# Optimization experiments

Measured on AMD Instinct MI355X. Metric: run time of the kernel, lower is better.

Reference implementation:

```python
import jax, jax.numpy as jnp
import numpy as np

B_SZ, L, D_MODEL = 2, 2048, 2048
INTER, HEADS, P, N, G, K = 4096, 64, 64, 128, 1, 4
CONV_DIM = INTER + 2 * G * N
EPS = 1e-5


def silu(x):
    return x * jax.nn.sigmoid(x)


def softplus_thresh(x, threshold=10.0):
    # matches source: where(x < thr, log(1+exp(x)), x)
    return jnp.where(x < threshold, jnp.log1p(jnp.exp(jnp.minimum(x, threshold))), x)


def setup_inputs() -> dict:
    key = jax.random.key(0)
    ks = jax.random.split(key, 8)
    s = 0.02
    return {
        "hidden_states": jax.random.normal(ks[0], (B_SZ, L, D_MODEL), jnp.float32),
        "W_z": jax.random.normal(ks[1], (D_MODEL, INTER), jnp.float32) * s,
        "W_xBC": jax.random.normal(ks[2], (D_MODEL, CONV_DIM), jnp.float32) * s,
        "W_dt": jax.random.normal(ks[3], (D_MODEL, HEADS), jnp.float32) * s,
        "conv_w": jax.random.normal(ks[4], (CONV_DIM, K), jnp.float32) * 0.1,
        "conv_b": jnp.zeros((CONV_DIM,), jnp.float32),
        "dt_bias": jax.random.uniform(ks[5], (HEADS,), jnp.float32, -2.0, 0.0),
        "A_log": jnp.log(jnp.arange(1, HEADS + 1, dtype=jnp.float32)),
        "D": jnp.ones((HEADS,), jnp.float32),
        "norm_w": jnp.ones((INTER,), jnp.float32),
        "W_out": jax.random.normal(ks[6], (INTER, D_MODEL), jnp.float32) * s,
    }


def reference(hidden_states, W_z, W_xBC, W_dt, conv_w, conv_b, dt_bias, A_log, D, norm_w, W_out):
    b, l, _ = hidden_states.shape
    Hg = HEADS // G  # heads per group

    gate = hidden_states @ W_z                      # [b,l,INTER]
    xBC = hidden_states @ W_xBC                     # [b,l,CONV_DIM]
    dt = softplus_thresh(hidden_states @ W_dt + dt_bias)  # [b,l,H]

    # causal depthwise conv1d + silu (padding=K-1, truncated to seq_len)
    xp = jnp.pad(xBC, ((0, 0), (K - 1, 0), (0, 0)))
    kern = jnp.transpose(conv_w)[:, None, :]        # [K,1,CONV_DIM] (WIO)
    xBC = jax.lax.conv_general_dilated(
        xp, kern, (1,), 'VALID',
        dimension_numbers=('NWC', 'WIO', 'NWC'),
        feature_group_count=CONV_DIM)
    xBC = silu(xBC + conv_b)

    gns = G * N
    x = xBC[..., :INTER].reshape(b, l, G, Hg, P)
    Bm = xBC[..., INTER:INTER + gns].reshape(b, l, G, N)
    Cm = xBC[..., INTER + gns:].reshape(b, l, G, N)

    A = -jnp.exp(A_log)                             # [H]
    dA = jnp.exp(dt * A).reshape(b, l, G, Hg)       # [b,l,G,Hg]
    dtx = dt.reshape(b, l, G, Hg)[..., None] * x    # [b,l,G,Hg,P]

    def step(state, inp):
        dA_t, dtx_t, B_t, C_t = inp
        # state: [b,G,Hg,P,N]
        state = state * dA_t[..., None, None] + dtx_t[..., None] * B_t[:, :, None, None, :]
        y_t = jnp.einsum('bghpn,bgn->bghp', state, C_t)
        return state, y_t

    xs = (jnp.moveaxis(dA, 1, 0), jnp.moveaxis(dtx, 1, 0),
          jnp.moveaxis(Bm, 1, 0), jnp.moveaxis(Cm, 1, 0))
    state0 = jnp.zeros((b, G, Hg, P, N), jnp.float32)
    _, ys = jax.lax.scan(step, state0, xs)          # [l,b,G,Hg,P]
    y = jnp.moveaxis(ys, 0, 1) + D.reshape(G, Hg)[..., None] * x
    scan_out = y.reshape(b, l, INTER)

    # gated RMSNorm within groups
    hs = scan_out.reshape(b, l, G, INTER // G).astype(jnp.float32)
    gt = gate.reshape(b, l, G, INTER // G).astype(jnp.float32)
    hs = hs * silu(gt)
    var = jnp.mean(hs * hs, axis=-1, keepdims=True)
    hs = hs * jax.lax.rsqrt(var + EPS)
    normed = norm_w * hs.reshape(b, l, INTER)

    return normed @ W_out
```

## Files before the change

### kernel.cpp

```cpp
#include <hip/hip_runtime.h>
#include <hip/hip_bf16.h>
#include <math.h>

typedef unsigned short u16;
typedef unsigned int   u32;
typedef __attribute__((ext_vector_type(8))) short short8;
typedef __attribute__((ext_vector_type(4))) float f32x4;

#define B_SZ     2
#define LSEQ     2048
#define DMODEL   2048
#define INTER    4096
#define HEADS    64
#define NSTATE   128
#define CONV_DIM 4352
#define XSTR     8576
#define NMAIN    8192
#define NTAILC   512
#define NTAILS   384
#define EPS      1e-5f
#define QCH      64
#define NCHUNK   (LSEQ / QCH)

__device__ __forceinline__ float bf2f(u16 u) {
    u32 v = ((u32)u) << 16;
    return __builtin_bit_cast(float, v);
}
__device__ __forceinline__ u16 f2bf(float x) {
    __hip_bfloat16 h = __float2bfloat16(x);
    return __builtin_bit_cast(u16, h);
}
__device__ __forceinline__ u32 pack2(float lo, float hi) {
    return (u32)f2bf(lo) | ((u32)f2bf(hi) << 16);
}
__device__ __forceinline__ void gl2lds16(const void* g, void* l) {
    __builtin_amdgcn_global_load_lds(
        (const __attribute__((address_space(1))) u32*)g,
        (__attribute__((address_space(3))) u32*)l, 16, 0, 0);
}

__global__ __launch_bounds__(256) void cvt_f32_bf16(
    const float* __restrict__ in, u16* __restrict__ out, int n4)
{
    int i = blockIdx.x * 256 + threadIdx.x;
    if (i >= n4) return;
    float4 v = ((const float4*)in)[i];
    ushort4 o;
    o.x = f2bf(v.x); o.y = f2bf(v.y); o.z = f2bf(v.z); o.w = f2bf(v.w);
    ((ushort4*)out)[i] = o;
}

__global__ __launch_bounds__(256) void tr_f32_bf16(
    const float* __restrict__ in, u16* __restrict__ out, int R, int C)
{
    __shared__ u16 tile[64][68];
    const int r0 = blockIdx.y * 64, c0 = blockIdx.x * 64;
    const int tr = threadIdx.x >> 4, tc = (threadIdx.x & 15) * 4;
    #pragma unroll
    for (int i = 0; i < 4; ++i) {
        int r = tr + i * 16;
        float4 v = *(const float4*)(in + (size_t)(r0 + r) * C + c0 + tc);
        tile[r][tc + 0] = f2bf(v.x);
        tile[r][tc + 1] = f2bf(v.y);
        tile[r][tc + 2] = f2bf(v.z);
        tile[r][tc + 3] = f2bf(v.w);
    }
    __syncthreads();
    #pragma unroll
    for (int i = 0; i < 4; ++i) {
        int oc = tr + i * 16;
        ushort4 o;
        o.x = tile[tc + 0][oc];
        o.y = tile[tc + 1][oc];
        o.z = tile[tc + 2][oc];
        o.w = tile[tc + 3][oc];
        *(ushort4*)(out + (size_t)(c0 + oc) * R + r0 + tc) = o;
    }
}

#define SA(c) (smem + (c) * 32768)
#define SB(c) (smem + (c) * 32768 + 16384)
#define STGA(c, q, ko) gl2lds16(gA + (size_t)((q) * 64) * lda + (ko), SA(c) + (q) * 4096 + lbase)
#define STGB(c, q, ko) gl2lds16(gB + (size_t)((q) * 64) * ldb + (ko), SB(c) + (q) * 4096 + lbase)

template<int OUT_BF16>
__global__ __launch_bounds__(512, 2) void gemm8(
    const u16* __restrict__ A, const u16* __restrict__ Bt, void* __restrict__ Co,
    int K, int lda, int ldb, int ldc, int Nstore)
{
    __shared__ __align__(16) u16 smem[65536];
    const int tid  = threadIdx.x;
    const int wave = tid >> 6, lane = tid & 63;
    const int wm = wave >> 2, wn = wave & 3;
    const int lr = lane & 15, lq = lane >> 4;

    const int nbx = gridDim.x;
    const int bid = blockIdx.y * nbx + blockIdx.x;
    const int nwg = nbx * gridDim.y;
    const int cpx = nwg >> 3;
    const int swz = (bid & 7) * cpx + (bid >> 3);
    const int n0 = (swz % nbx) * 256;
    const int m0 = (swz / nbx) * 256;
    const int kbase = blockIdx.z * K;

    const int srow  = tid >> 3;
    const int scb8  = ((tid & 7) ^ (srow & 7)) << 3;
    const int lbase = (tid >> 6) << 9;
    const u16* gA = A  + (size_t)(m0 + srow) * lda + kbase + scb8;
    const u16* gB = Bt + (size_t)(n0 + srow) * ldb + kbase + scb8;

    f32x4 acc[8][4];
    #pragma unroll
    for (int i = 0; i < 8; ++i)
        #pragma unroll
        for (int j = 0; j < 4; ++j) acc[i][j] = (f32x4)0.f;

    const int nt = K >> 6;

    STGA(0, 0, 0); STGA(0, 1, 0); STGA(0, 2, 0); STGA(0, 3, 0);
    STGB(0, 0, 0); STGB(0, 1, 0); STGB(0, 2, 0); STGB(0, 3, 0);
    __builtin_amdgcn_sched_barrier(0);
    asm volatile("s_waitcnt vmcnt(0)" ::: "memory");
    __builtin_amdgcn_s_barrier();

    for (int t = 0; t < nt; ++t) {
        const int c = t & 1;
        if (t + 1 < nt) {
            const int k1 = (t + 1) << 6;
            STGA(c ^ 1, 0, k1); STGA(c ^ 1, 1, k1);
            STGA(c ^ 1, 2, k1); STGA(c ^ 1, 3, k1);
            STGB(c ^ 1, 0, k1); STGB(c ^ 1, 1, k1);
            STGB(c ^ 1, 2, k1); STGB(c ^ 1, 3, k1);
        }
        __builtin_amdgcn_sched_barrier(0);
        const u16* Ab = SA(c);
        const u16* Bb = SB(c);
        #pragma unroll
        for (int kk = 0; kk < 2; ++kk) {
            short8 a8[8], b4[4];
            #pragma unroll
            for (int i = 0; i < 8; ++i)
                a8[i] = *(const short8*)(Ab + (wm * 128 + i * 16 + lr) * 64
                                         + ((((kk) * 4 + lq) ^ (lr & 7)) << 3));
            #pragma unroll
            for (int j = 0; j < 4; ++j)
                b4[j] = *(const short8*)(Bb + (wn * 64 + j * 16 + lr) * 64
                                         + ((((kk) * 4 + lq) ^ (lr & 7)) << 3));
            __builtin_amdgcn_s_setprio(1);
            #pragma unroll
            for (int i = 0; i < 8; ++i)
                #pragma unroll
                for (int j = 0; j < 4; ++j)
                    acc[i][j] = __builtin_amdgcn_mfma_f32_16x16x32_bf16(
                        a8[i], b4[j], acc[i][j], 0, 0, 0);
            __builtin_amdgcn_s_setprio(0);
        }
        if (t + 1 < nt) {
            asm volatile("s_waitcnt vmcnt(0)" ::: "memory");
            __builtin_amdgcn_s_barrier();
        }
    }

    const int odd = lr & 1;
    const bool wstore = (n0 + wn * 64) < Nstore;
    #pragma unroll
    for (int i = 0; i < 8; ++i)
        #pragma unroll
        for (int j = 0; j < 4; ++j) {
            float v0 = acc[i][j][0], v1 = acc[i][j][1];
            float v2 = acc[i][j][2], v3 = acc[i][j][3];
            float n0v = __shfl_xor(v0, 1), n1v = __shfl_xor(v1, 1);
            float n2v = __shfl_xor(v2, 1), n3v = __shfl_xor(v3, 1);
            int colb  = n0 + wn * 64 + j * 16 + (lr & ~1);
            int rbase = m0 + wm * 128 + i * 16 + lq * 4 + odd * 2;
            if (wstore) {
                if (OUT_BF16) {
                    u32 w0 = odd ? pack2(n2v, v2) : pack2(v0, n0v);
                    u32 w1 = odd ? pack2(n3v, v3) : pack2(v1, n1v);
                    *(u32*)((u16*)Co + (size_t)rbase * ldc + colb) = w0;
                    *(u32*)((u16*)Co + (size_t)(rbase + 1) * ldc + colb) = w1;
                } else {
                    float* Cf = (float*)Co + (size_t)blockIdx.z * 4096 * ldc;
                    float2 f0 = odd ? make_float2(n2v, v2) : make_float2(v0, n0v);
                    float2 f1 = odd ? make_float2(n3v, v3) : make_float2(v1, n1v);
                    *(float2*)(Cf + (size_t)rbase * ldc + colb) = f0;
                    *(float2*)(Cf + (size_t)(rbase + 1) * ldc + colb) = f1;
                }
            }
        }
}

__global__ __launch_bounds__(256) void tail_add(
    const float* __restrict__ Pt, u16* __restrict__ xall_)
{
    int i = blockIdx.x * 256 + threadIdx.x;
    int row = i / 96, cq = (i % 96) * 4;
    const float* p = Pt + (size_t)row * NTAILC + cq;
    const size_t zs = (size_t)4096 * NTAILC;
    float4 a = *(const float4*)(p);
    float4 b = *(const float4*)(p + zs);
    float4 c = *(const float4*)(p + 2 * zs);
    float4 d = *(const float4*)(p + 3 * zs);
    ushort4 o;
    o.x = f2bf(a.x + b.x + c.x + d.x);
    o.y = f2bf(a.y + b.y + c.y + d.y);
    o.z = f2bf(a.z + b.z + c.z + d.z);
    o.w = f2bf(a.w + b.w + c.w + d.w);
    *(ushort4*)(xall_ + (size_t)row * XSTR + NMAIN + cq) = o;
}

__global__ __launch_bounds__(256) void add2_f32(
    const float* __restrict__ a, const float* __restrict__ b,
    float* __restrict__ o, int n4)
{
    int i = blockIdx.x * 256 + threadIdx.x;
    if (i >= n4) return;
    float4 x = ((const float4*)a)[i];
    float4 y = ((const float4*)b)[i];
    x.x += y.x; x.y += y.y; x.z += y.z; x.w += y.w;
    ((float4*)o)[i] = x;
}

__global__ void dt_kernel(const u16* __restrict__ xall,
                          float* __restrict__ dtb,
                          const float* __restrict__ dt_bias, int n)
{
    int i = blockIdx.x * 256 + threadIdx.x;
    if (i >= n) return;
    int h = i & 63, row = i >> 6;
    float x = bf2f(xall[(size_t)row * XSTR + INTER + CONV_DIM + h]) + dt_bias[h];
    dtb[i] = (x < 10.f) ? log1pf(expf(x)) : x;
}

__global__ __launch_bounds__(256) void conv_kernel(
    const u16* __restrict__ xall, const float* __restrict__ cw,
    const float* __restrict__ cb, u16* __restrict__ xout)
{
    int c4 = blockIdx.x * 256 + threadIdx.x;
    if (c4 >= CONV_DIM / 4) return;
    int c  = c4 * 4;
    int bt = blockIdx.y;
    int t  = bt & (LSEQ - 1);
    const u16* xi = xall + (size_t)bt * XSTR + INTER + c;
    float4 w0 = *(const float4*)(cw + (size_t)(c + 0) * 4);
    float4 w1 = *(const float4*)(cw + (size_t)(c + 1) * 4);
    float4 w2 = *(const float4*)(cw + (size_t)(c + 2) * 4);
    float4 w3 = *(const float4*)(cw + (size_t)(c + 3) * 4);
    float4 bb = *(const float4*)(cb + c);
    float a0 = bb.x, a1 = bb.y, a2 = bb.z, a3 = bb.w;
    ushort4 x0 = *(const ushort4*)(xi);
    a0 = fmaf(bf2f(x0.x), w0.w, a0); a1 = fmaf(bf2f(x0.y), w1.w, a1);
    a2 = fmaf(bf2f(x0.z), w2.w, a2); a3 = fmaf(bf2f(x0.w), w3.w, a3);
    if (t >= 1) {
        ushort4 xm = *(const ushort4*)(xi - XSTR);
        a0 = fmaf(bf2f(xm.x), w0.z, a0); a1 = fmaf(bf2f(xm.y), w1.z, a1);
        a2 = fmaf(bf2f(xm.z), w2.z, a2); a3 = fmaf(bf2f(xm.w), w3.z, a3);
    }
    if (t >= 2) {
        ushort4 xm = *(const ushort4*)(xi - 2 * XSTR);
        a0 = fmaf(bf2f(xm.x), w0.y, a0); a1 = fmaf(bf2f(xm.y), w1.y, a1);
        a2 = fmaf(bf2f(xm.z), w2.y, a2); a3 = fmaf(bf2f(xm.w), w3.y, a3);
    }
    if (t >= 3) {
        ushort4 xm = *(const ushort4*)(xi - 3 * XSTR);
        a0 = fmaf(bf2f(xm.x), w0.x, a0); a1 = fmaf(bf2f(xm.y), w1.x, a1);
        a2 = fmaf(bf2f(xm.z), w2.x, a2); a3 = fmaf(bf2f(xm.w), w3.x, a3);
    }
    ushort4 o;
    o.x = f2bf(a0 / (1.f + expf(-a0)));
    o.y = f2bf(a1 / (1.f + expf(-a1)));
    o.z = f2bf(a2 / (1.f + expf(-a2)));
    o.w = f2bf(a3 / (1.f + expf(-a3)));
    *(ushort4*)(xout + (size_t)bt * CONV_DIM + c) = o;
}

__global__ __launch_bounds__(256) void ssd_chunk_state(
    const u16* __restrict__ xc, const float* __restrict__ dtb,
    const float* __restrict__ A_log,
    u16* __restrict__ Tg, float* __restrict__ decayQ)
{
    const int bid = blockIdx.x;
    const int b = bid >> 11, h = (bid >> 5) & 63, c = bid & 31;
    const int t0 = c * QCH;
    const int tid = threadIdx.x;
    const int wave = tid >> 6, lane = tid & 63;
    const int lr = lane & 15, lq = lane >> 4;

    __shared__ __align__(16) u16 BT[128][72];
    __shared__ __align__(16) u16 XwT[64][72];
    __shared__ float sclL[QCH];

    const u16* xg = xc + (size_t)b * LSEQ * CONV_DIM;

    if (tid < 64) {
        float dtv = dtb[((size_t)b * LSEQ + t0 + tid) * HEADS + h];
        float a = -dtv * expf(A_log[h]);
        float s = a;
        #pragma unroll
        for (int off = 1; off < 64; off <<= 1) {
            float o = __shfl_up(s, off, 64);
            if (tid >= off) s += o;
        }
        float cq = __shfl(s, 63, 64);
        sclL[tid] = dtv * expf(cq - s);
        if (tid == 0) decayQ[((b * 64 + h) << 5) + c] = expf(cq);
    }
    __syncthreads();

    #pragma unroll
    for (int r = 0; r < 16; ++r) {
        int idx = tid + 256 * r, j = idx >> 6, p = idx & 63;
        float v = bf2f(xg[(size_t)(t0 + j) * CONV_DIM + h * 64 + p]);
        XwT[p][j] = f2bf(v * sclL[j]);
    }
    #pragma unroll
    for (int r = 0; r < 32; ++r) {
        int idx = tid + 256 * r, j = idx >> 7, n = idx & 127;
        BT[n][j] = xg[(size_t)(t0 + j) * CONV_DIM + INTER + n];
    }
    __syncthreads();

    f32x4 acc[8];
    #pragma unroll
    for (int i = 0; i < 8; ++i) acc[i] = (f32x4)0.f;
    #pragma unroll
    for (int k0 = 0; k0 < QCH; k0 += 32) {
        short8 af = *(const short8*)&XwT[wave * 16 + lr][k0 + lq * 8];
        #pragma unroll
        for (int nt = 0; nt < 8; ++nt) {
            short8 bfr = *(const short8*)&BT[nt * 16 + lr][k0 + lq * 8];
            acc[nt] = __builtin_amdgcn_mfma_f32_16x16x32_bf16(af, bfr, acc[nt], 0, 0, 0);
        }
    }
    u16* To = Tg + ((((size_t)(b * 64 + h)) * NCHUNK + c) * 64) * 128;
    #pragma unroll
    for (int nt = 0; nt < 8; ++nt)
        #pragma unroll
        for (int r = 0; r < 4; ++r)
            To[(wave * 16 + lq * 4 + r) * 128 + nt * 16 + lr] = f2bf(acc[nt][r]);
}

__global__ __launch_bounds__(256) void ssd_state_scan(
    u16* __restrict__ Tg, const float* __restrict__ decayQ)
{
    const int bh = blockIdx.x >> 2, nq = blockIdx.x & 3;
    const int tid = threadIdx.x;
    const int p = tid >> 2, nb = nq * 32 + (tid & 3) * 8;
    float S[8];
    #pragma unroll
    for (int m = 0; m < 8; ++m) S[m] = 0.f;

    for (int c = 0; c < NCHUNK; ++c) {
        u16* base = Tg + ((((size_t)bh * NCHUNK + c) * 64 + p) * 128) + nb;
        uint4 tv = *(const uint4*)base;
        uint4 sv;
        sv.x = pack2(S[0], S[1]);
        sv.y = pack2(S[2], S[3]);
        sv.z = pack2(S[4], S[5]);
        sv.w = pack2(S[6], S[7]);
        *(uint4*)base = sv;
        float dq = decayQ[(bh << 5) + c];
        const u32* w = (const u32*)&tv;
        #pragma unroll
        for (int e = 0; e < 4; ++e) {
            S[e*2]     = fmaf(dq, S[e*2],     bf2f((u16)(w[e] & 0xffffu)));
            S[e*2 + 1] = fmaf(dq, S[e*2 + 1], bf2f((u16)(w[e] >> 16)));
        }
    }
}

__global__ __launch_bounds__(256) void ssd_output(
    const u16* __restrict__ xc, const float* __restrict__ dtb,
    const float* __restrict__ A_log, const float* __restrict__ Dvec,
    const u16* __restrict__ Sg,
    u16* __restrict__ y)
{
    const int bid = blockIdx.x;
    const int b = bid >> 11, h = (bid >> 5) & 63, c = bid & 31;
    const int t0 = c * QCH;
    const int tid = threadIdx.x;
    const int wave = tid >> 6, lane = tid & 63;
    const int lr = lane & 15, lq = lane >> 4;

    __shared__ __align__(16) u16 C_lds[64][136];
    __shared__ __align__(16) u16 B_lds[64][136];
    __shared__ __align__(16) u16 S_lds[64][136];
    __shared__ __align__(16) u16 P_lds[64][72];
    __shared__ __align__(16) u16 XT[64][72];
    __shared__ float cumL[QCH], dtsL[QCH], escL[QCH];

    const u16* xg = xc + (size_t)b * LSEQ * CONV_DIM;

    if (tid < 64) {
        float dtv = dtb[((size_t)b * LSEQ + t0 + tid) * HEADS + h];
        float a = -dtv * expf(A_log[h]);
        float s = a;
        #pragma unroll
        for (int off = 1; off < 64; off <<= 1) {
            float o = __shfl_up(s, off, 64);
            if (tid >= off) s += o;
        }
        cumL[tid] = s;
        dtsL[tid] = dtv;
        escL[tid] = expf(s);
    }
    #pragma unroll
    for (int r4 = 0; r4 < 4; ++r4) {
        int idx4 = tid + 256 * r4;
        int j = idx4 >> 4, c8 = (idx4 & 15) * 8;
        *(uint4*)&B_lds[j][c8] = *(const uint4*)(xg + (size_t)(t0 + j) * CONV_DIM + INTER + c8);
        *(uint4*)&C_lds[j][c8] = *(const uint4*)(xg + (size_t)(t0 + j) * CONV_DIM + INTER + NSTATE + c8);
        *(uint4*)&S_lds[j][c8] = *(const uint4*)(Sg + ((((size_t)(b * 64 + h)) * NCHUNK + c) * 64 + j) * 128 + c8);
    }
    #pragma unroll
    for (int r = 0; r < 16; ++r) {
        int idx = tid + 256 * r, j = idx >> 6, p = idx & 63;
        XT[p][j] = xg[(size_t)(t0 + j) * CONV_DIM + h * 64 + p];
    }
    __syncthreads();

    f32x4 accG[4];
    #pragma unroll
    for (int i = 0; i < 4; ++i) accG[i] = (f32x4)0.f;
    #pragma unroll
    for (int k0 = 0; k0 < NSTATE; k0 += 32) {
        short8 af = *(const short8*)&C_lds[wave * 16 + lr][k0 + lq * 8];
        #pragma unroll
        for (int jt = 0; jt < 4; ++jt) {
            short8 bfr = *(const short8*)&B_lds[jt * 16 + lr][k0 + lq * 8];
            accG[jt] = __builtin_amdgcn_mfma_f32_16x16x32_bf16(af, bfr, accG[jt], 0, 0, 0);
        }
    }
    #pragma unroll
    for (int jt = 0; jt < 4; ++jt)
        #pragma unroll
        for (int r = 0; r < 4; ++r) {
            int ii = wave * 16 + lq * 4 + r;
            int jj = jt * 16 + lr;
            float v = (jj <= ii)
                ? accG[jt][r] * dtsL[jj] * expf(cumL[ii] - cumL[jj]) : 0.f;
            P_lds[ii][jj] = f2bf(v);
        }
    __syncthreads();

    f32x4 accY[4], accZ[4];
    #pragma unroll
    for (int i = 0; i < 4; ++i) { accY[i] = (f32x4)0.f; accZ[i] = (f32x4)0.f; }
    #pragma unroll
    for (int k0 = 0; k0 < QCH; k0 += 32) {
        short8 af = *(const short8*)&P_lds[wave * 16 + lr][k0 + lq * 8];
        #pragma unroll
        for (int pt = 0; pt < 4; ++pt) {
            short8 bfr = *(const short8*)&XT[pt * 16 + lr][k0 + lq * 8];
            accY[pt] = __builtin_amdgcn_mfma_f32_16x16x32_bf16(af, bfr, accY[pt], 0, 0, 0);
        }
    }
    #pragma unroll
    for (int k0 = 0; k0 < NSTATE; k0 += 32) {
        short8 af = *(const short8*)&C_lds[wave * 16 + lr][k0 + lq * 8];
        #pragma unroll
        for (int pt = 0; pt < 4; ++pt) {
            short8 bfr = *(const short8*)&S_lds[pt * 16 + lr][k0 + lq * 8];
            accZ[pt] = __builtin_amdgcn_mfma_f32_16x16x32_bf16(af, bfr, accZ[pt], 0, 0, 0);
        }
    }

    const float Dh = Dvec[h];
    u16* yg = y + ((size_t)b * LSEQ + t0) * XSTR + h * 64;
    #pragma unroll
    for (int pt = 0; pt < 4; ++pt)
        #pragma unroll
        for (int r = 0; r < 4; ++r) {
            int ii = wave * 16 + lq * 4 + r;
            int pp = pt * 16 + lr;
            float xv = bf2f(XT[pp][ii]);
            float o = accY[pt][r] + escL[ii] * accZ[pt][r] + Dh * xv;
            yg[(size_t)ii * XSTR + pp] = f2bf(o);
        }
}

__global__ __launch_bounds__(256) void norm_kernel(
    u16* __restrict__ xall, const float* __restrict__ w)
{
    const int row = blockIdx.x;
    const u16* yr = xall + (size_t)row * XSTR + INTER;
    u16*       gr = xall + (size_t)row * XSTR;
    const int tid = threadIdx.x;

    float v[16];
    float ss = 0.f;
    #pragma unroll
    for (int i = 0; i < 2; ++i) {
        int e0 = i * 2048 + tid * 8;
        uint4 hv4 = *(const uint4*)(yr + e0);
        uint4 gv4 = *(const uint4*)(gr + e0);
        const u16* hp = (const u16*)&hv4;
        const u16* gp = (const u16*)&gv4;
        #pragma unroll
        for (int k = 0; k < 8; ++k) {
            float hv = bf2f(hp[k]);
            float g  = bf2f(gp[k]);
            float val = hv * (g / (1.f + expf(-g)));
            v[i * 8 + k] = val;
            ss = fmaf(val, val, ss);
        }
    }
    #pragma unroll
    for (int o = 32; o > 0; o >>= 1) ss += __shfl_xor(ss, o);
    __shared__ float part[4];
    if ((tid & 63) == 0) part[tid >> 6] = ss;
    __syncthreads();
    float tot  = part[0] + part[1] + part[2] + part[3];
    float rinv = rsqrtf(tot * (1.f / INTER) + EPS);
    #pragma unroll
    for (int i = 0; i < 2; ++i) {
        int e0 = i * 2048 + tid * 8;
        float4 wa = *(const float4*)(w + e0);
        float4 wb = *(const float4*)(w + e0 + 4);
        uint4 sv;
        sv.x = pack2(wa.x * v[i*8+0] * rinv, wa.y * v[i*8+1] * rinv);
        sv.y = pack2(wa.z * v[i*8+2] * rinv, wa.w * v[i*8+3] * rinv);
        sv.z = pack2(wb.x * v[i*8+4] * rinv, wb.y * v[i*8+5] * rinv);
        sv.w = pack2(wb.z * v[i*8+6] * rinv, wb.w * v[i*8+7] * rinv);
        *(uint4*)(gr + e0) = sv;
    }
}

extern "C" void kernel_launch(void* const* d_in, const int* in_sizes, int n_in,
                              void* d_out, int out_size, void* d_ws, size_t ws_size,
                              hipStream_t stream)
{
    const float* hs      = (const float*)d_in[0];
    const float* W_z     = (const float*)d_in[1];
    const float* W_xBC   = (const float*)d_in[2];
    const float* W_dt    = (const float*)d_in[3];
    const float* conv_w  = (const float*)d_in[4];
    const float* conv_b  = (const float*)d_in[5];
    const float* dt_bias = (const float*)d_in[6];
    const float* A_log   = (const float*)d_in[7];
    const float* Dv      = (const float*)d_in[8];
    const float* norm_w  = (const float*)d_in[9];
    const float* W_out   = (const float*)d_in[10];
    float* out = (float*)d_out;
    char*  w8  = (char*)d_ws;

    u16* hs_bf  = (u16*)(w8 + 0);
    u16* Wt_all = (u16*)(w8 + 16777216);
    u16* Tbuf   = (u16*)(w8 + 0);
    float* Cpart= (float*)(w8 + 0);
    u16* Wt_out = (u16*)(w8 + 67108864);
    u16* xall   = (u16*)(w8 + 83886080);
    u16* xconv  = (u16*)(w8 + 154140672);
    float* Ptail= (float*)(w8 + 154140672);
    float* dtb  = (float*)(w8 + 189792256);
    float* dcq  = (float*)(w8 + 190840832);

    const int M = B_SZ * LSEQ;

    cvt_f32_bf16<<<(M * DMODEL / 4 + 255) / 256, 256, 0, stream>>>(hs, hs_bf, M * DMODEL / 4);
    tr_f32_bf16<<<dim3(INTER / 64,    DMODEL / 64), 256, 0, stream>>>(W_z,   Wt_all, DMODEL, INTER);
    tr_f32_bf16<<<dim3(CONV_DIM / 64, DMODEL / 64), 256, 0, stream>>>(W_xBC, Wt_all + (size_t)INTER * DMODEL, DMODEL, CONV_DIM);
    tr_f32_bf16<<<dim3(1,             DMODEL / 64), 256, 0, stream>>>(W_dt,  Wt_all + (size_t)(INTER + CONV_DIM) * DMODEL, DMODEL, 64);
    hipMemsetAsync(Wt_all + (size_t)(INTER + CONV_DIM + 64) * DMODEL, 0, (size_t)192 * DMODEL * 2, stream);
    tr_f32_bf16<<<dim3(DMODEL / 64,   INTER / 64),  256, 0, stream>>>(W_out, Wt_out, INTER, DMODEL);

    gemm8<1><<<dim3(NMAIN / 256, M / 256, 1), 512, 0, stream>>>(
        hs_bf, Wt_all, (void*)xall, DMODEL , DMODEL, DMODEL,
        XSTR , NMAIN );
    gemm8<0><<<dim3(NTAILC / 256, M / 256, 4), 512, 0, stream>>>(
        hs_bf, Wt_all + (size_t)NMAIN * DMODEL, (void*)Ptail, DMODEL / 4 ,
        DMODEL, DMODEL, NTAILC , NTAILS );
    tail_add<<<M * (NTAILS / 4) / 256, 256, 0, stream>>>(Ptail, xall);

    dt_kernel<<<(M * HEADS + 255) / 256, 256, 0, stream>>>(xall, dtb, dt_bias, M * HEADS);
    conv_kernel<<<dim3((CONV_DIM / 4 + 255) / 256, M), 256, 0, stream>>>(xall, conv_w, conv_b, xconv);

    ssd_chunk_state<<<B_SZ * HEADS * NCHUNK, 256, 0, stream>>>(xconv, dtb, A_log, Tbuf, dcq);
    ssd_state_scan<<<B_SZ * HEADS * 4, 256, 0, stream>>>(Tbuf, dcq);
    ssd_output<<<B_SZ * HEADS * NCHUNK, 256, 0, stream>>>(xconv, dtb, A_log, Dv, Tbuf, xall + INTER);

    norm_kernel<<<M, 256, 0, stream>>>(xall, norm_w);

    gemm8<0><<<dim3(DMODEL / 256, M / 256, 2), 512, 0, stream>>>(
        xall, Wt_out, (void*)Cpart, INTER / 2 , XSTR ,
        INTER , DMODEL , DMODEL );
    add2_f32<<<(M * DMODEL / 4 + 255) / 256, 256, 0, stream>>>(
        Cpart, Cpart + (size_t)M * DMODEL, out, M * DMODEL / 4);
}
```

Before: 624.0 us.

## Restructure GEMM mainloop into phased interleaved loads; fuse dt into conv; vectorize SSD loads

The GEMM mainloop is split into four phases per K tile. Each phase issues a subset of the next-tile global-to-LDS stages between MFMA groups, and A halves are prefetched two tiles ahead with partial vmcnt waits, so memory traffic overlaps compute instead of being issued all at once. The dt softplus kernel is folded into spare threads of the conv kernel, removing one launch. The transposed LDS fills in the SSD kernels now use 16-byte vector global loads instead of scalar loads. The phased loop adds more barriers and assumes an even tile count.

New measurement: 631.1 us. Within noise of the previous version (+1.1%).

```diff
diff --git a/kernel.cpp b/kernel.cpp
--- a/kernel.cpp
+++ b/kernel.cpp
@@ -5,6 +5,7 @@
 typedef unsigned short u16;
 typedef unsigned int   u32;
 typedef __attribute__((ext_vector_type(8))) short short8;
+typedef __attribute__((ext_vector_type(8))) unsigned short us8;
 typedef __attribute__((ext_vector_type(4))) float f32x4;
 
 #define B_SZ     2
@@ -83,6 +84,52 @@
 #define STGA(c, q, ko) gl2lds16(gA + (size_t)((q) * 64) * lda + (ko), SA(c) + (q) * 4096 + lbase)
 #define STGB(c, q, ko) gl2lds16(gB + (size_t)((q) * 64) * ldb + (ko), SB(c) + (q) * 4096 + lbase)
 
+#define PH(mh, kk, READB, STAGES, TAIL)                                          \
+  {                                                                              \
+    short8 af[4];                                                                \
+    _Pragma("unroll")                                                            \
+    for (int i_ = 0; i_ < 4; ++i_)                                               \
+      af[i_] = *(const short8*)(Ab + (wm * 128 + (mh) * 64 + i_ * 16 + lr) * 64  \
+                                + ((((kk) * 4 + lq) ^ (lr & 7)) << 3));          \
+    if (READB) {                                                                 \
+      _Pragma("unroll")                                                          \
+      for (int j_ = 0; j_ < 4; ++j_)                                             \
+        bfr[kk][j_] = *(const short8*)(Bb + (wn * 64 + j_ * 16 + lr) * 64        \
+                                       + ((((kk) * 4 + lq) ^ (lr & 7)) << 3));   \
+    }                                                                            \
+    STAGES                                                                       \
+    __builtin_amdgcn_sched_barrier(0);                                           \
+    __builtin_amdgcn_s_barrier();                                                \
+    asm volatile("s_waitcnt lgkmcnt(0)" ::: "memory");                           \
+    __builtin_amdgcn_sched_barrier(0);                                           \
+    __builtin_amdgcn_s_setprio(1);                                               \
+    _Pragma("unroll")                                                            \
+    for (int i_ = 0; i_ < 4; ++i_)                                               \
+      _Pragma("unroll")                                                          \
+      for (int j_ = 0; j_ < 4; ++j_)                                             \
+        acc[(mh) * 4 + i_][j_] = __builtin_amdgcn_mfma_f32_16x16x32_bf16(        \
+            af[i_], bfr[kk][j_], acc[(mh) * 4 + i_][j_], 0, 0, 0);               \
+    __builtin_amdgcn_s_setprio(0);                                               \
+    __builtin_amdgcn_sched_barrier(0);                                           \
+    TAIL                                                                         \
+    __builtin_amdgcn_s_barrier();                                                \
+  }
+
+#define TILE(tt, c)                                                              \
+  {                                                                              \
+    const int t_ = (tt);                                                         \
+    const int k1_ = (t_ + 1) << 6, k2_ = (t_ + 2) << 6;                          \
+    const bool st1_ = (t_ + 1 < nt), st2_ = (t_ + 2 < nt);                       \
+    const u16* Ab = SA(c); const u16* Bb = SB(c);                                \
+    PH(0, 0, 1, { if (st1_) { STGA((c) ^ 1, 1, k1_); STGA((c) ^ 1, 3, k1_); } }, {}) \
+    PH(1, 0, 0, { if (st1_) { STGB((c) ^ 1, 0, k1_); STGB((c) ^ 1, 1, k1_); } }, {}) \
+    PH(0, 1, 1, { if (st1_) { STGB((c) ^ 1, 2, k1_); STGB((c) ^ 1, 3, k1_); } }, {}) \
+    PH(1, 1, 0, { if (st2_) { STGA((c), 0, k2_); STGA((c), 2, k2_); } },         \
+       { if (t_ < nt - 1) {                                                      \
+           if (st2_) { asm volatile("s_waitcnt vmcnt(2)" ::: "memory"); }        \
+           else      { asm volatile("s_waitcnt vmcnt(0)" ::: "memory"); } } })   \
+  }
+
 template<int OUT_BF16>
 __global__ __launch_bounds__(512, 2) void gemm8(
     const u16* __restrict__ A, const u16* __restrict__ Bt, void* __restrict__ Co,
@@ -114,51 +161,21 @@
     for (int i = 0; i < 8; ++i)
         #pragma unroll
         for (int j = 0; j < 4; ++j) acc[i][j] = (f32x4)0.f;
+    short8 bfr[2][4];
 
     const int nt = K >> 6;
 
     STGA(0, 0, 0); STGA(0, 1, 0); STGA(0, 2, 0); STGA(0, 3, 0);
     STGB(0, 0, 0); STGB(0, 1, 0); STGB(0, 2, 0); STGB(0, 3, 0);
+    STGA(1, 0, 64); STGA(1, 2, 64);
     __builtin_amdgcn_sched_barrier(0);
-    asm volatile("s_waitcnt vmcnt(0)" ::: "memory");
+    asm volatile("s_waitcnt vmcnt(2)" ::: "memory");
+    __builtin_amdgcn_sched_barrier(0);
     __builtin_amdgcn_s_barrier();
 
-    for (int t = 0; t < nt; ++t) {
-        const int c = t & 1;
-        if (t + 1 < nt) {
-            const int k1 = (t + 1) << 6;
-            STGA(c ^ 1, 0, k1); STGA(c ^ 1, 1, k1);
-            STGA(c ^ 1, 2, k1); STGA(c ^ 1, 3, k1);
-            STGB(c ^ 1, 0, k1); STGB(c ^ 1, 1, k1);
-            STGB(c ^ 1, 2, k1); STGB(c ^ 1, 3, k1);
-        }
-        __builtin_amdgcn_sched_barrier(0);
-        const u16* Ab = SA(c);
-        const u16* Bb = SB(c);
-        #pragma unroll
-        for (int kk = 0; kk < 2; ++kk) {
-            short8 a8[8], b4[4];
-            #pragma unroll
-            for (int i = 0; i < 8; ++i)
-                a8[i] = *(const short8*)(Ab + (wm * 128 + i * 16 + lr) * 64
-                                         + ((((kk) * 4 + lq) ^ (lr & 7)) << 3));
-            #pragma unroll
-            for (int j = 0; j < 4; ++j)
-                b4[j] = *(const short8*)(Bb + (wn * 64 + j * 16 + lr) * 64
-                                         + ((((kk) * 4 + lq) ^ (lr & 7)) << 3));
-            __builtin_amdgcn_s_setprio(1);
-            #pragma unroll
-            for (int i = 0; i < 8; ++i)
-                #pragma unroll
-                for (int j = 0; j < 4; ++j)
-                    acc[i][j] = __builtin_amdgcn_mfma_f32_16x16x32_bf16(
-                        a8[i], b4[j], acc[i][j], 0, 0, 0);
-            __builtin_amdgcn_s_setprio(0);
-        }
-        if (t + 1 < nt) {
-            asm volatile("s_waitcnt vmcnt(0)" ::: "memory");
-            __builtin_amdgcn_s_barrier();
-        }
+    for (int t = 0; t < nt; t += 2) {
+        TILE(t, 0)
+        TILE(t + 1, 1)
     }
 
     const int odd = lr & 1;
@@ -221,25 +238,22 @@
     ((float4*)o)[i] = x;
 }
 
-__global__ void dt_kernel(const u16* __restrict__ xall,
-                          float* __restrict__ dtb,
-                          const float* __restrict__ dt_bias, int n)
-{
-    int i = blockIdx.x * 256 + threadIdx.x;
-    if (i >= n) return;
-    int h = i & 63, row = i >> 6;
-    float x = bf2f(xall[(size_t)row * XSTR + INTER + CONV_DIM + h]) + dt_bias[h];
-    dtb[i] = (x < 10.f) ? log1pf(expf(x)) : x;
-}
-
 __global__ __launch_bounds__(256) void conv_kernel(
     const u16* __restrict__ xall, const float* __restrict__ cw,
-    const float* __restrict__ cb, u16* __restrict__ xout)
+    const float* __restrict__ cb, u16* __restrict__ xout,
+    float* __restrict__ dtb, const float* __restrict__ dt_bias)
 {
     int c4 = blockIdx.x * 256 + threadIdx.x;
-    if (c4 >= CONV_DIM / 4) return;
+    int bt = blockIdx.y;
+    if (c4 >= CONV_DIM / 4) {
+        int h = c4 - CONV_DIM / 4;
+        if (h < HEADS) {
+            float x = bf2f(xall[(size_t)bt * XSTR + INTER + CONV_DIM + h]) + dt_bias[h];
+            dtb[bt * HEADS + h] = (x < 10.f) ? log1pf(expf(x)) : x;
+        }
+        return;
+    }
     int c  = c4 * 4;
-    int bt = blockIdx.y;
     int t  = bt & (LSEQ - 1);
     const u16* xi = xall + (size_t)bt * XSTR + INTER + c;
     float4 w0 = *(const float4*)(cw + (size_t)(c + 0) * 4);
@@ -308,15 +322,23 @@
     __syncthreads();
 
     #pragma unroll
-    for (int r = 0; r < 16; ++r) {
-        int idx = tid + 256 * r, j = idx >> 6, p = idx & 63;
-        float v = bf2f(xg[(size_t)(t0 + j) * CONV_DIM + h * 64 + p]);
-        XwT[p][j] = f2bf(v * sclL[j]);
-    }
-    #pragma unroll
-    for (int r = 0; r < 32; ++r) {
-        int idx = tid + 256 * r, j = idx >> 7, n = idx & 127;
-        BT[n][j] = xg[(size_t)(t0 + j) * CONV_DIM + INTER + n];
+    for (int r = 0; r < 2; ++r) {
+        int idx = tid + 256 * r;
+        int j = idx >> 3, p8 = (idx & 7) * 8;
+        us8 xv = *(const us8*)(xg + (size_t)(t0 + j) * CONV_DIM + h * 64 + p8);
+        float scl = sclL[j];
+        #pragma unroll
+        for (int k = 0; k < 8; ++k)
+            XwT[p8 + k][j] = f2bf(bf2f(xv[k]) * scl);
+    }
+    #pragma unroll
+    for (int r = 0; r < 4; ++r) {
+        int idx = tid + 256 * r;
+        int j = idx >> 4, n8 = (idx & 15) * 8;
+        us8 bv = *(const us8*)(xg + (size_t)(t0 + j) * CONV_DIM + INTER + n8);
+        #pragma unroll
+        for (int k = 0; k < 8; ++k)
+            BT[n8 + k][j] = bv[k];
     }
     __syncthreads();
 
@@ -413,9 +435,13 @@
         *(uint4*)&S_lds[j][c8] = *(const uint4*)(Sg + ((((size_t)(b * 64 + h)) * NCHUNK + c) * 64 + j) * 128 + c8);
     }
     #pragma unroll
-    for (int r = 0; r < 16; ++r) {
-        int idx = tid + 256 * r, j = idx >> 6, p = idx & 63;
-        XT[p][j] = xg[(size_t)(t0 + j) * CONV_DIM + h * 64 + p];
+    for (int r = 0; r < 2; ++r) {
+        int idx = tid + 256 * r;
+        int j = idx >> 3, p8 = (idx & 7) * 8;
+        us8 xv = *(const us8*)(xg + (size_t)(t0 + j) * CONV_DIM + h * 64 + p8);
+        #pragma unroll
+        for (int k = 0; k < 8; ++k)
+            XT[p8 + k][j] = xv[k];
     }
     __syncthreads();
 
@@ -572,8 +598,8 @@
         DMODEL, DMODEL, NTAILC , NTAILS );
     tail_add<<<M * (NTAILS / 4) / 256, 256, 0, stream>>>(Ptail, xall);
 
-    dt_kernel<<<(M * HEADS + 255) / 256, 256, 0, stream>>>(xall, dtb, dt_bias, M * HEADS);
-    conv_kernel<<<dim3((CONV_DIM / 4 + 255) / 256, M), 256, 0, stream>>>(xall, conv_w, conv_b, xconv);
+    conv_kernel<<<dim3((CONV_DIM / 4 + 255) / 256, M), 256, 0, stream>>>(
+        xall, conv_w, conv_b, xconv, dtb, dt_bias);
 
     ssd_chunk_state<<<B_SZ * HEADS * NCHUNK, 256, 0, stream>>>(xconv, dtb, A_log, Tbuf, dcq);
     ssd_state_scan<<<B_SZ * HEADS * 4, 256, 0, stream>>>(Tbuf, dcq);
```
